# Kernel tuning notes

Measured on AMD Instinct MI355X. Metric: run time of the kernel, lower is better.

The kernel has to match this reference:

```python
import jax, jax.numpy as jnp
import numpy as np

B, L, DQ, DK, NH = 32, 2048, 1024, 1024, 16
DH = DK // NH  # per-head dim = 64

def setup_inputs() -> dict:
    key = jax.random.key(0)
    ks = jax.random.split(key, 8)
    sq = np.sqrt(2.0 / (DQ + DH)).astype(np.float32)
    sk = np.sqrt(2.0 / (DK + DH)).astype(np.float32)
    return {
        "q": jax.random.normal(ks[0], (B, DQ), jnp.float32),
        "k": jax.random.normal(ks[1], (B, L, DK), jnp.float32),
        "Wq": jax.random.normal(ks[2], (NH * DH, DQ), jnp.float32) * sq,
        "bq": jnp.zeros((NH * DH,), jnp.float32),
        "Wk": jax.random.normal(ks[3], (NH * DH, DK), jnp.float32) * sk,
        "bk": jnp.zeros((NH * DH,), jnp.float32),
        "Wv": jax.random.normal(ks[4], (NH * DH, DK), jnp.float32) * sk,
        "bv": jnp.zeros((NH * DH,), jnp.float32),
    }

def reference(q, k, Wq, bq, Wk, bk, Wv, bv):
    # projections (standard GEMMs), reshape to heads
    qs = (q @ Wq.T + bq).reshape(B, NH, DH)            # [b,n,dh]
    ksr = (k @ Wk.T + bk).reshape(B, L, NH, DH)        # [b,l,n,dh]
    vs = (k @ Wv.T + bv).reshape(B, L, NH, DH)         # [b,l,n,dh]
    temp = jnp.sqrt(jnp.asarray(DH, qs.dtype))
    # single-query attention scores per head, softmax over l
    attn = jnp.einsum('bnd,blnd->bnl', qs, ksr) / temp  # [b,n,l]
    attn = jax.nn.softmax(attn, axis=-1)
    out = jnp.einsum('bnl,blnd->bnd', attn, vs).reshape(B, NH * DH)
    # original returns attn flattened as (n_head*b, l) with head-major order
    attn_flat = jnp.transpose(attn, (1, 0, 2)).reshape(NH * B, L)
    return out, attn_flat
```

## Files before the change

kernel.cpp:

```cpp
#include <hip/hip_runtime.h>
#include <hip/hip_bf16.h>

#define NB 32
#define NL 2048
#define ND 1024
#define NHH 16
#define NDH 64

typedef __bf16 bf16;
typedef __attribute__((ext_vector_type(4))) __bf16 bf16x4;
typedef __attribute__((ext_vector_type(8))) __bf16 bf16x8;
typedef __attribute__((ext_vector_type(4))) float f32x4;

#define SBAR __builtin_amdgcn_s_barrier()
#define WAIT_LGKM0 asm volatile("s_waitcnt lgkmcnt(0)" ::: "memory")
#define WAIT_VM0 asm volatile("s_waitcnt vmcnt(0)" ::: "memory")

#define SWZ(r) (((r) & 7) << 4)

__device__ __forceinline__ float dot4(float4 a, float4 b) {
  return a.x * b.x + a.y * b.y + a.z * b.z + a.w * b.w;
}

__global__ __launch_bounds__(256) void qs_kernel(
    const float* __restrict__ q, const float* __restrict__ Wq,
    const float* __restrict__ bq, float* __restrict__ qs) {
  int o = blockIdx.x;
  int lane = threadIdx.x & 63;
  int wv = threadIdx.x >> 6;
  const float4* wrow = reinterpret_cast<const float4*>(Wq + (size_t)o * ND) + lane * 4;
  float4 w0 = wrow[0], w1 = wrow[1], w2 = wrow[2], w3 = wrow[3];
#pragma unroll
  for (int bb = 0; bb < 8; ++bb) {
    int b = wv * 8 + bb;
    const float4* qr = reinterpret_cast<const float4*>(q + (size_t)b * ND) + lane * 4;
    float s = dot4(qr[0], w0) + dot4(qr[1], w1) + dot4(qr[2], w2) + dot4(qr[3], w3);
#pragma unroll
    for (int off = 32; off > 0; off >>= 1) s += __shfl_down(s, off, 64);
    if (lane == 0) qs[(size_t)b * ND + o] = s + bq[o];
  }
}

__global__ __launch_bounds__(256) void qt_kernel(
    const float* __restrict__ Wk, const float* __restrict__ qs,
    float* __restrict__ qt) {
  int n  = blockIdx.x >> 4;
  int ic = (blockIdx.x >> 2) & 3;
  int bg = blockIdx.x & 3;
  int i = ic * 256 + threadIdx.x;
  __shared__ float s_qs[8][64];
  for (int t = threadIdx.x; t < 512; t += 256) {
    int b = t >> 6, d = t & 63;
    s_qs[b][d] = qs[(size_t)(bg * 8 + b) * ND + n * NDH + d];
  }
  __syncthreads();
  float acc[8];
#pragma unroll
  for (int b = 0; b < 8; ++b) acc[b] = 0.f;
  for (int d = 0; d < 64; ++d) {
    float w = Wk[((size_t)(n * NDH + d)) * ND + i];
#pragma unroll
    for (int b = 0; b < 8; ++b) acc[b] += w * s_qs[b][d];
  }
#pragma unroll
  for (int b = 0; b < 8; ++b)
    qt[((size_t)((bg * 8 + b) * NHH + n)) * ND + i] = acc[b];
}

__global__ __launch_bounds__(256) void qb_kernel(
    const float* __restrict__ qs, const float* __restrict__ bk,
    float* __restrict__ qb) {
  int t = blockIdx.x * 256 + threadIdx.x;
  if (t >= 512) return;
  int b = t >> 4, n = t & 15;
  float s = 0.f;
  for (int d = 0; d < 64; ++d)
    s += qs[(size_t)b * ND + n * NDH + d] * bk[n * NDH + d];
  qb[t] = s;
}

__global__ __launch_bounds__(512, 4) void fused_kernel(
    const float* __restrict__ kin, const float* __restrict__ qt,
    const float* __restrict__ qb, float* __restrict__ attn,
    float* __restrict__ ctxp) {
  int bx = blockIdx.x;
  int b  = bx >> 4;
  int sl = bx & 15;
  int tid = threadIdx.x, lane = tid & 63, wv = tid >> 6;
  int kg = lane >> 4, ln16 = lane & 15;

  __shared__ __align__(16) float kbf[2][8][1024];
  __shared__ __align__(16) float pbuf[8][8][20];
  __shared__ __align__(16) float sP[8][20];

  bf16x8 afrag[4];
  {
    const float* qrow = qt + ((size_t)(b * NHH + ln16)) * ND + wv * 128 + kg * 8;
#pragma unroll
    for (int mm = 0; mm < 4; ++mm) {
      f32x4 f0 = *reinterpret_cast<const f32x4*>(qrow + mm * 32);
      f32x4 f1 = *reinterpret_cast<const f32x4*>(qrow + mm * 32 + 4);
      bf16x8 v;
      v[0] = (bf16)f0[0]; v[1] = (bf16)f0[1]; v[2] = (bf16)f0[2]; v[3] = (bf16)f0[3];
      v[4] = (bf16)f1[0]; v[5] = (bf16)f1[1]; v[6] = (bf16)f1[2]; v[7] = (bf16)f1[3];
      afrag[mm] = v;
    }
  }

  int rl = tid & 7, rn = tid >> 3;
  float qbv = (tid < 128) ? qb[b * NHH + rn] : 0.f;

  int nh = tid >> 8, ic = tid & 255;
  f32x4 ctxa[8];
#pragma unroll
  for (int r = 0; r < 8; ++r) ctxa[r] = (f32x4){0.f, 0.f, 0.f, 0.f};

  int sw = SWZ(wv);
  const char* krow0 =
      (const char*)(kin + ((size_t)(b * NL + sl * 128 + wv)) * ND);

#define DMA_TILE(TT, BB)                                                    \
  {                                                                         \
    const char* gsrc = krow0 + (size_t)(TT) * 8 * 4096;                     \
    char* ldst = (char*)kbf + (BB) * 32768 + wv * 4096;                     \
    _Pragma("unroll")                                                       \
    for (int j = 0; j < 4; ++j) {                                           \
      int gb = (j * 1024 + lane * 16) ^ sw;                                 \
      __builtin_amdgcn_global_load_lds(                                     \
          (const unsigned int*)(gsrc + gb),                                 \
          (unsigned int*)(ldst + j * 1024), 16, 0, 0);                      \
    }                                                                       \
  }

  DMA_TILE(0, 0)
  WAIT_VM0;
  SBAR;

  for (int t = 0; t < 16; ++t) {
    int cur = t & 1;
    const char* kbc = (const char*)kbf + cur * 32768;

    if (t < 15) DMA_TILE(t + 1, cur ^ 1)

    {
      int arow = ln16 & 7;
      int swA = SWZ(arow);
      const char* rb = kbc + arow * 4096;
      f32x4 acc = {0.f, 0.f, 0.f, 0.f};
#pragma unroll
      for (int mm = 0; mm < 4; ++mm) {
        int kcb = (wv * 128 + mm * 32 + kg * 8) * 4;
        f32x4 f0 = *reinterpret_cast<const f32x4*>(rb + (kcb ^ swA));
        f32x4 f1 = *reinterpret_cast<const f32x4*>(rb + (kcb ^ swA ^ 16));
        bf16x8 bfr;
        bfr[0] = (bf16)f0[0]; bfr[1] = (bf16)f0[1];
        bfr[2] = (bf16)f0[2]; bfr[3] = (bf16)f0[3];
        bfr[4] = (bf16)f1[0]; bfr[5] = (bf16)f1[1];
        bfr[6] = (bf16)f1[2]; bfr[7] = (bf16)f1[3];
        acc = __builtin_amdgcn_mfma_f32_16x16x32_bf16(afrag[mm], bfr, acc, 0, 0, 0);
      }
      if (ln16 < 8)
        *reinterpret_cast<f32x4*>(&pbuf[wv][ln16][kg * 4]) = acc;
    }
    WAIT_LGKM0;
    SBAR;

    if (tid < 128) {
      float s = 0.f;
#pragma unroll
      for (int w = 0; w < 8; ++w) s += pbuf[w][rl][rn];
      float p = __expf((s + qbv) * 0.125f);
      sP[rl][rn] = p;
      attn[((size_t)(rn * NB + b)) * NL + sl * 128 + t * 8 + rl] = p;
    }
    WAIT_LGKM0;
    SBAR;

#pragma unroll
    for (int l = 0; l < 8; ++l) {
      const char* rb = kbc + l * 4096;
      f32x4 kf = *reinterpret_cast<const f32x4*>(rb + ((ic * 16) ^ SWZ(l)));
      f32x4 p0 = *reinterpret_cast<const f32x4*>(&sP[l][nh * 8]);
      f32x4 p1 = *reinterpret_cast<const f32x4*>(&sP[l][nh * 8 + 4]);
#pragma unroll
      for (int n = 0; n < 4; ++n) {
        ctxa[n]     += p0[n] * kf;
        ctxa[4 + n] += p1[n] * kf;
      }
    }

    WAIT_VM0;
    WAIT_LGKM0;
    SBAR;
  }
#undef DMA_TILE

#pragma unroll
  for (int n = 0; n < 8; ++n) {
    float* dst = ctxp + (((size_t)sl * NB + b) * NHH + nh * 8 + n) * ND + ic * 4;
    *reinterpret_cast<f32x4*>(dst) = ctxa[n];
  }
}

__global__ __launch_bounds__(256) void norm_kernel(float* __restrict__ attn,
                                                   float* __restrict__ invS) {
  int row = blockIdx.x;
  float* p = attn + (size_t)row * NL;
  int tid = threadIdx.x;
  int lane = tid & 63, wv = tid >> 6;
  float v[8];
  float s = 0.f;
#pragma unroll
  for (int j = 0; j < 8; ++j) {
    v[j] = p[tid + j * 256];
    s += v[j];
  }
#pragma unroll
  for (int off = 32; off > 0; off >>= 1) s += __shfl_down(s, off, 64);
  __shared__ float ss[4];
  if (lane == 0) ss[wv] = s;
  __syncthreads();
  float inv = 1.f / (ss[0] + ss[1] + ss[2] + ss[3]);
  if (tid == 0) invS[row] = inv;
#pragma unroll
  for (int j = 0; j < 8; ++j) p[tid + j * 256] = v[j] * inv;
}

__global__ __launch_bounds__(256) void reduce_kernel(
    const float* __restrict__ ctxp, float* __restrict__ ctx) {
  size_t e4 = ((size_t)blockIdx.x * 256 + threadIdx.x) * 4;
  f32x4 s = *reinterpret_cast<const f32x4*>(ctxp + e4);
#pragma unroll
  for (int sl = 1; sl < 16; ++sl)
    s += *reinterpret_cast<const f32x4*>(ctxp + (size_t)sl * NB * NHH * ND + e4);
  *reinterpret_cast<f32x4*>(ctx + e4) = s;
}

__global__ __launch_bounds__(256) void out_kernel(
    const float* __restrict__ Wv, const float* __restrict__ bv,
    const float* __restrict__ ctx, const float* __restrict__ invS,
    float* __restrict__ out) {
  int o = blockIdx.x;
  int n = o >> 6;
  int lane = threadIdx.x & 63;
  int wv = threadIdx.x >> 6;
  const float4* wrow = reinterpret_cast<const float4*>(Wv + (size_t)o * ND) + lane * 4;
  float4 w0 = wrow[0], w1 = wrow[1], w2 = wrow[2], w3 = wrow[3];
#pragma unroll
  for (int bb = 0; bb < 8; ++bb) {
    int b = wv * 8 + bb;
    const float4* cr =
        reinterpret_cast<const float4*>(ctx + ((size_t)(b * NHH + n)) * ND) + lane * 4;
    float s = dot4(cr[0], w0) + dot4(cr[1], w1) + dot4(cr[2], w2) + dot4(cr[3], w3);
#pragma unroll
    for (int off = 32; off > 0; off >>= 1) s += __shfl_down(s, off, 64);
    if (lane == 0) out[(size_t)b * ND + o] = s * invS[n * NB + b] + bv[o];
  }
}

extern "C" void kernel_launch(void* const* d_in, const int* in_sizes, int n_in,
                              void* d_out, int out_size, void* d_ws, size_t ws_size,
                              hipStream_t stream) {
  const float* q  = (const float*)d_in[0];
  const float* k  = (const float*)d_in[1];
  const float* Wq = (const float*)d_in[2];
  const float* bq = (const float*)d_in[3];
  const float* Wk = (const float*)d_in[4];
  const float* bk = (const float*)d_in[5];
  const float* Wv = (const float*)d_in[6];
  const float* bv = (const float*)d_in[7];

  float* out  = (float*)d_out;
  float* attn = out + NB * ND;

  float* ws   = (float*)d_ws;
  float* qs   = ws;
  float* qt   = ws + 32768;
  float* qb   = qt + 524288;
  float* invS = qb + 512;
  float* ctx  = invS + 512;
  float* ctxp = ctx + 524288;

  qs_kernel<<<1024, 256, 0, stream>>>(q, Wq, bq, qs);
  qt_kernel<<<256, 256, 0, stream>>>(Wk, qs, qt);
  qb_kernel<<<2, 256, 0, stream>>>(qs, bk, qb);
  fused_kernel<<<512, 512, 0, stream>>>(k, qt, qb, attn, ctxp);
  norm_kernel<<<512, 256, 0, stream>>>(attn, invS);
  reduce_kernel<<<512, 256, 0, stream>>>(ctxp, ctx);
  out_kernel<<<1024, 256, 0, stream>>>(Wv, bv, ctx, invS, out);
}
```

Before: 110.1 us.

## Software-pipeline fused attention loop across three stages with deeper K buffering

Restructures the fused kernel's tile loop into a skewed three-stage pipeline. In each iteration it issues the DMA for tile t+2, computes MFMA scores for tile t+1, runs exp/softmax for tile t, and accumulates context for tile t-1, so only one barrier is needed per iteration instead of three. It uses four K buffers and double-buffered score and probability scratch to make this safe. The grid is also halved so each block covers 256 rows of L, which halves the partial-context writes and the reduce work. The costs are 128KB of LDS per block, which likely limits occupancy to one block per CU, and only 256 blocks to fill the device.

```diff
diff --git a/kernel.cpp b/kernel.cpp
--- a/kernel.cpp
+++ b/kernel.cpp
@@ -84,14 +84,14 @@
     const float* __restrict__ qb, float* __restrict__ attn,
     float* __restrict__ ctxp) {
   int bx = blockIdx.x;
-  int b  = bx >> 4;
-  int sl = bx & 15;
+  int b  = bx >> 3;
+  int sl = bx & 7;
   int tid = threadIdx.x, lane = tid & 63, wv = tid >> 6;
   int kg = lane >> 4, ln16 = lane & 15;
 
-  __shared__ __align__(16) float kbf[2][8][1024];
-  __shared__ __align__(16) float pbuf[8][8][20];
-  __shared__ __align__(16) float sP[8][20];
+  __shared__ __align__(16) float kbf[4][8][1024];
+  __shared__ __align__(16) float pbuf[2][8][8][20];
+  __shared__ __align__(16) float sP[2][8][20];
 
   bf16x8 afrag[4];
   {
@@ -117,7 +117,7 @@
 
   int sw = SWZ(wv);
   const char* krow0 =
-      (const char*)(kin + ((size_t)(b * NL + sl * 128 + wv)) * ND);
+      (const char*)(kin + ((size_t)(b * NL + sl * 256 + wv)) * ND);
 
 #define DMA_TILE(TT, BB)                                                    \
   {                                                                         \
@@ -133,16 +133,16 @@
   }
 
   DMA_TILE(0, 0)
-  WAIT_VM0;
-  SBAR;
-
-  for (int t = 0; t < 16; ++t) {
-    int cur = t & 1;
-    const char* kbc = (const char*)kbf + cur * 32768;
-
-    if (t < 15) DMA_TILE(t + 1, cur ^ 1)
-
-    {
+
+  for (int t = -1; t <= 32; ++t) {
+    WAIT_VM0;
+    WAIT_LGKM0;
+    SBAR;
+
+    if (t + 2 <= 31) DMA_TILE(t + 2, (t + 2) & 3)
+
+    if (t + 1 <= 31) {
+      const char* kbc = (const char*)kbf + ((t + 1) & 3) * 32768;
       int arow = ln16 & 7;
       int swA = SWZ(arow);
       const char* rb = kbc + arow * 4096;
@@ -160,38 +160,34 @@
         acc = __builtin_amdgcn_mfma_f32_16x16x32_bf16(afrag[mm], bfr, acc, 0, 0, 0);
       }
       if (ln16 < 8)
-        *reinterpret_cast<f32x4*>(&pbuf[wv][ln16][kg * 4]) = acc;
-    }
-    WAIT_LGKM0;
-    SBAR;
-
-    if (tid < 128) {
+        *reinterpret_cast<f32x4*>(&pbuf[(t + 1) & 1][wv][ln16][kg * 4]) = acc;
+    }
+
+    if (t >= 0 && t <= 31 && tid < 128) {
       float s = 0.f;
 #pragma unroll
-      for (int w = 0; w < 8; ++w) s += pbuf[w][rl][rn];
+      for (int w = 0; w < 8; ++w) s += pbuf[t & 1][w][rl][rn];
       float p = __expf((s + qbv) * 0.125f);
-      sP[rl][rn] = p;
-      attn[((size_t)(rn * NB + b)) * NL + sl * 128 + t * 8 + rl] = p;
-    }
-    WAIT_LGKM0;
-    SBAR;
-
-#pragma unroll
-    for (int l = 0; l < 8; ++l) {
-      const char* rb = kbc + l * 4096;
-      f32x4 kf = *reinterpret_cast<const f32x4*>(rb + ((ic * 16) ^ SWZ(l)));
-      f32x4 p0 = *reinterpret_cast<const f32x4*>(&sP[l][nh * 8]);
-      f32x4 p1 = *reinterpret_cast<const f32x4*>(&sP[l][nh * 8 + 4]);
-#pragma unroll
-      for (int n = 0; n < 4; ++n) {
-        ctxa[n]     += p0[n] * kf;
-        ctxa[4 + n] += p1[n] * kf;
+      sP[t & 1][rl][rn] = p;
+      attn[((size_t)(rn * NB + b)) * NL + sl * 256 + t * 8 + rl] = p;
+    }
+
+    if (t >= 1) {
+      const char* kbc = (const char*)kbf + ((t - 1) & 3) * 32768;
+      const float* sp = &sP[(t - 1) & 1][0][0];
+#pragma unroll
+      for (int l = 0; l < 8; ++l) {
+        const char* rb = kbc + l * 4096;
+        f32x4 kf = *reinterpret_cast<const f32x4*>(rb + ((ic * 16) ^ SWZ(l)));
+        f32x4 p0 = *reinterpret_cast<const f32x4*>(sp + l * 20 + nh * 8);
+        f32x4 p1 = *reinterpret_cast<const f32x4*>(sp + l * 20 + nh * 8 + 4);
+#pragma unroll
+        for (int n = 0; n < 4; ++n) {
+          ctxa[n]     += p0[n] * kf;
+          ctxa[4 + n] += p1[n] * kf;
+        }
       }
     }
-
-    WAIT_VM0;
-    WAIT_LGKM0;
-    SBAR;
   }
 #undef DMA_TILE
 
@@ -231,7 +227,7 @@
   size_t e4 = ((size_t)blockIdx.x * 256 + threadIdx.x) * 4;
   f32x4 s = *reinterpret_cast<const f32x4*>(ctxp + e4);
 #pragma unroll
-  for (int sl = 1; sl < 16; ++sl)
+  for (int sl = 1; sl < 8; ++sl)
     s += *reinterpret_cast<const f32x4*>(ctxp + (size_t)sl * NB * NHH * ND + e4);
   *reinterpret_cast<f32x4*>(ctx + e4) = s;
 }
@@ -284,7 +280,7 @@
   qs_kernel<<<1024, 256, 0, stream>>>(q, Wq, bq, qs);
   qt_kernel<<<256, 256, 0, stream>>>(Wk, qs, qt);
   qb_kernel<<<2, 256, 0, stream>>>(qs, bk, qb);
-  fused_kernel<<<512, 512, 0, stream>>>(k, qt, qb, attn, ctxp);
+  fused_kernel<<<256, 512, 0, stream>>>(k, qt, qb, attn, ctxp);
   norm_kernel<<<512, 256, 0, stream>>>(attn, invS);
   reduce_kernel<<<512, 256, 0, stream>>>(ctxp, ctx);
   out_kernel<<<1024, 256, 0, stream>>>(Wv, bv, ctx, invS, out);
```

New measurement: 100.7 us. -8.6%, faster.
